# Optimization experiments

Measured on AMD Instinct MI355X. Metric: run time of the kernel, lower is better.

## Reference

```python
import jax, jax.numpy as jnp
from jax import lax
import numpy as np


def _run_lstm(x, W, U, b, reverse=False):
    # x: [B,T,I]; W: [I,4U]; U: [U,4U]; b: [4U]; Keras gate order i,f,g,o
    # activation='relu' (candidate and cell-output), recurrent_activation=sigmoid
    if reverse:
        x = x[:, ::-1]
    u = U.shape[0]
    xz = jnp.einsum('bti,ij->btj', x, W) + b  # precompute input projection

    def step(carry, z_t):
        h, c = carry
        z = z_t + h @ U
        i, f, g, o = jnp.split(z, 4, axis=-1)
        i = jax.nn.sigmoid(i)
        f = jax.nn.sigmoid(f)
        g = jax.nn.relu(g)
        o = jax.nn.sigmoid(o)
        c = f * c + i * g
        h = o * jax.nn.relu(c)
        return (h, c), h

    B = x.shape[0]
    init = (jnp.zeros((B, u), x.dtype), jnp.zeros((B, u), x.dtype))
    _, hs = lax.scan(step, init, jnp.swapaxes(xz, 0, 1))
    hs = jnp.swapaxes(hs, 0, 1)  # [B,T,U]
    if reverse:
        hs = hs[:, ::-1]  # Keras Bidirectional re-reverses backward output
    return hs


def _bilstm(x, Wf, Uf, bf, Wb, Ub, bb):
    return jnp.concatenate([_run_lstm(x, Wf, Uf, bf, False),
                            _run_lstm(x, Wb, Ub, bb, True)], axis=-1)


def _forward(x, p):
    (e1fW, e1fU, e1fb, e1bW, e1bU, e1bb,
     e2fW, e2fU, e2fb, e2bW, e2bU, e2bb,
     d1fW, d1fU, d1fb, d1bW, d1bU, d1bb,
     d2fW, d2fU, d2fb, d2bW, d2bU, d2bb,
     Wd, bd) = p
    T = x.shape[1]
    h = _bilstm(x, e1fW, e1fU, e1fb, e1bW, e1bU, e1bb)          # [B,T,2N]
    # encoder lstm2: return_sequences=False -> last fwd state, last bwd state
    fwd = _run_lstm(h, e2fW, e2fU, e2fb, False)[:, -1]           # [B,N/2]
    bwd = _run_lstm(h, e2bW, e2bU, e2bb, True)[:, 0]             # [B,N/2]
    z = jnp.concatenate([fwd, bwd], axis=-1)                     # [B,N]
    z = jnp.broadcast_to(z[:, None, :], (z.shape[0], T, z.shape[1]))  # RepeatVector
    h = _bilstm(z, d1fW, d1fU, d1fb, d1bW, d1bU, d1bb)           # [B,T,N]
    h = _bilstm(h, d2fW, d2fU, d2fb, d2bW, d2bU, d2bb)           # [B,T,2N]
    return jnp.einsum('btd,df->btf', h, Wd) + bd                 # TimeDistributed Dense


def setup_inputs():
    B, T, F, N = 512, 256, 64, 128
    ks = iter(jax.random.split(jax.random.key(0), 40))

    def p(shape, s=0.05):
        return jax.random.normal(next(ks), shape, jnp.float32) * s

    def cell(ind, u):
        # Keras defaults: zero bias with unit forget-gate bias
        b = jnp.zeros((4 * u,), jnp.float32).at[u:2 * u].set(1.0)
        return p((ind, 4 * u)), p((u, 4 * u)), b

    d = {'x': jax.random.normal(next(ks), (B, T, F), jnp.float32)}
    for name, ind, u in [('e1', F, N), ('e2', 2 * N, N // 2), ('d1', N, N // 2), ('d2', N, N)]:
        for dr in ('f', 'b'):
            W, U, b = cell(ind, u)
            d[name + dr + '_W'] = W
            d[name + dr + '_U'] = U
            d[name + dr + '_b'] = b
    d['Wd'] = p((2 * N, F))
    d['bd'] = jnp.zeros((F,), jnp.float32)
    return d


def reference(x, e1f_W, e1f_U, e1f_b, e1b_W, e1b_U, e1b_b,
              e2f_W, e2f_U, e2f_b, e2b_W, e2b_U, e2b_b,
              d1f_W, d1f_U, d1f_b, d1b_W, d1b_U, d1b_b,
              d2f_W, d2f_U, d2f_b, d2b_W, d2b_U, d2b_b, Wd, bd):
    return _forward(x, (e1f_W, e1f_U, e1f_b, e1b_W, e1b_U, e1b_b,
                        e2f_W, e2f_U, e2f_b, e2b_W, e2b_U, e2b_b,
                        d1f_W, d1f_U, d1f_b, d1b_W, d1b_U, d1b_b,
                        d2f_W, d2f_U, d2f_b, d2b_W, d2b_U, d2b_b, Wd, bd))
```

## Files before the change

### kernel.cpp

```cpp
#include <hip/hip_runtime.h>


#define THREADS 512

using f32x4 = __attribute__((ext_vector_type(4))) float;
using bfrag = __attribute__((ext_vector_type(8))) short;

__device__ __forceinline__ float sigf(float x) { return 1.0f / (1.0f + __expf(-x)); }
__device__ __forceinline__ unsigned short f2bf(float f) {
    unsigned u = __float_as_uint(f);
    u += 0x7FFFu + ((u >> 16) & 1u);
    return (unsigned short)(u >> 16);
}
__device__ __forceinline__ float bf2f(unsigned short h) {
    return __uint_as_float(((unsigned)h) << 16);
}
__device__ __forceinline__ int fragw(int kc, int r) {
    return ((kc * 16 + r) ^ (kc & 7)) * 8;
}

template<int UH, int XK, bool LASTONLY>
__global__ __launch_bounds__(THREADS, 2)
void lstm_rec(const float* __restrict__ xz, const size_t xz_ds, const size_t xz_ss,
              const float* __restrict__ xin,
              const float* __restrict__ Uf, const float* __restrict__ Ub,
              const float* __restrict__ Wf, const float* __restrict__ Wb,
              const float* __restrict__ bf, const float* __restrict__ bb,
              float* __restrict__ out,
              float* __restrict__ stc, float* __restrict__ sth,
              const int T, const int t0, const int TCc, const int FIRST, const int LASTC)
{
    constexpr int NCOL = 4 * UH;
    constexpr int NS   = NCOL / 8;
    constexpr int NT   = NS / 16;
    constexpr int KT   = UH / 32;
    constexpr int XKT  = XK / 32;
    constexpr int PPT  = 16 * UH / THREADS;
    constexpr int BQS  = THREADS / UH;
    constexpr int ZP   = NCOL + 4;
    static_assert(XK == 0 || XK == 64, "x path");
    static_assert(NT >= 1 && KT >= 1 && PPT >= 1, "shape");

    const int dir = blockIdx.y;
    const bool rev = (dir != 0);
    const float* __restrict__ U  = dir ? Ub : Uf;
    const float* __restrict__ Wm = dir ? Wb : Wf;
    const float* __restrict__ bs = dir ? bb : bf;

    const int b0  = blockIdx.x * 16;
    const int tid = threadIdx.x;
    const int wv  = tid >> 6;
    const int l   = tid & 63;
    const int lr  = l & 15;
    const int kg  = l >> 4;
    const int c0  = wv * NS;

    __shared__ unsigned short hh_hi[UH * 16], hh_lo[UH * 16];
    __shared__ unsigned short xh_hi[XK > 0 ? 2 * XK * 16 : 8];
    __shared__ unsigned short xh_lo[XK > 0 ? 2 * XK * 16 : 8];
    __shared__ float zs[16 * ZP];

    bfrag whi[NT][KT], wlo[NT][KT];
    #pragma unroll
    for (int nt = 0; nt < NT; ++nt)
        #pragma unroll
        for (int kt = 0; kt < KT; ++kt) {
            const int col = c0 + nt * 16 + lr;
            #pragma unroll
            for (int i = 0; i < 8; ++i) {
                const int k = kt * 32 + kg * 8 + i;
                const float w = U[(size_t)k * NCOL + col];
                const unsigned short h = f2bf(w);
                whi[nt][kt][i] = (short)h;
                wlo[nt][kt][i] = (short)f2bf(w - bf2f(h));
            }
        }
    bfrag wxhi[NT][XKT > 0 ? XKT : 1];
    float biasr[NT];
    if constexpr (XK > 0) {
        #pragma unroll
        for (int nt = 0; nt < NT; ++nt) {
            const int col = c0 + nt * 16 + lr;
            #pragma unroll
            for (int kt = 0; kt < XKT; ++kt)
                #pragma unroll
                for (int i = 0; i < 8; ++i)
                    wxhi[nt][kt][i] = (short)f2bf(Wm[(size_t)(kt * 32 + kg * 8 + i) * NCOL + col]);
            biasr[nt] = bs[col];
        }
    }

    const int ut = tid % UH;
    float cst[PPT];

    if (FIRST) {
        for (int i = tid; i < UH * 16; i += THREADS) { hh_hi[i] = 0; hh_lo[i] = 0; }
        #pragma unroll
        for (int q = 0; q < PPT; ++q) cst[q] = 0.0f;
    } else {
        #pragma unroll
        for (int q = 0; q < PPT; ++q) {
            const int b = tid / UH + q * BQS;
            const float hv = sth[((size_t)dir * 512 + b0 + b) * UH + ut];
            const unsigned short hi = f2bf(hv);
            const unsigned short lo = f2bf(hv - bf2f(hi));
            hh_hi[fragw(ut >> 3, b) + (ut & 7)] = hi;
            hh_lo[fragw(ut >> 3, b) + (ut & 7)] = lo;
            cst[q] = stc[((size_t)dir * 512 + b0 + b) * UH + ut];
        }
    }
    if constexpr (XK > 0) {
        const int gt0 = rev ? (T - 1 - t0) : t0;
        const int bb = tid >> 5, f = (tid & 31) * 2;
        const float2 xv = *(const float2*)&xin[((size_t)(b0 + bb) * T + gt0) * XK + f];
        const unsigned short h0 = f2bf(xv.x), h1 = f2bf(xv.y);
        const unsigned short l0 = f2bf(xv.x - bf2f(h0)), l1 = f2bf(xv.y - bf2f(h1));
        const int off = fragw(f >> 3, bb) + (f & 7);
        *(unsigned*)&xh_hi[off] = (unsigned)h0 | ((unsigned)h1 << 16);
        *(unsigned*)&xh_lo[off] = (unsigned)l0 | ((unsigned)l1 << 16);
    }
    __syncthreads();

    for (int p = 0; p < TCc; ++p) {
        const int gt = rev ? (T - 1 - (t0 + p)) : (t0 + p);

        float2 xnext;
        const bool havex = (XK > 0) && (p + 1 < TCc);
        if (havex) {
            const int gtn = rev ? (T - 1 - (t0 + p + 1)) : (t0 + p + 1);
            const int bb = tid >> 5, f = (tid & 31) * 2;
            xnext = *(const float2*)&xin[((size_t)(b0 + bb) * T + gtn) * XK + f];
        }
        float xzr[PPT][4];
        if constexpr (XK == 0) {
            const float* xrow = xz + (size_t)dir * xz_ds + (size_t)p * xz_ss;
            #pragma unroll
            for (int q = 0; q < PPT; ++q) {
                const int b = tid / UH + q * BQS;
                const float* r = xrow + (size_t)(b0 + b) * NCOL + ut;
                #pragma unroll
                for (int g = 0; g < 4; ++g) xzr[q][g] = r[g * UH];
            }
        }

        f32x4 acc[NT];
        #pragma unroll
        for (int nt = 0; nt < NT; ++nt) {
            if constexpr (XK > 0) acc[nt] = f32x4{biasr[nt], biasr[nt], biasr[nt], biasr[nt]};
            else                  acc[nt] = f32x4{0.f, 0.f, 0.f, 0.f};
        }
        #pragma unroll
        for (int kt = 0; kt < KT; ++kt) {
            const bfrag ahi = *(const bfrag*)&hh_hi[fragw(kt * 4 + kg, lr)];
            const bfrag alo = *(const bfrag*)&hh_lo[fragw(kt * 4 + kg, lr)];
            #pragma unroll
            for (int nt = 0; nt < NT; ++nt) {
                acc[nt] = __builtin_amdgcn_mfma_f32_16x16x32_bf16(ahi, whi[nt][kt], acc[nt], 0, 0, 0);
                acc[nt] = __builtin_amdgcn_mfma_f32_16x16x32_bf16(alo, whi[nt][kt], acc[nt], 0, 0, 0);
                acc[nt] = __builtin_amdgcn_mfma_f32_16x16x32_bf16(ahi, wlo[nt][kt], acc[nt], 0, 0, 0);
            }
        }
        if constexpr (XK > 0) {
            const int xb = (p & 1) * XK * 16;
            #pragma unroll
            for (int kt = 0; kt < XKT; ++kt) {
                const bfrag xhi = *(const bfrag*)&xh_hi[xb + fragw(kt * 4 + kg, lr)];
                const bfrag xlo = *(const bfrag*)&xh_lo[xb + fragw(kt * 4 + kg, lr)];
                #pragma unroll
                for (int nt = 0; nt < NT; ++nt) {
                    acc[nt] = __builtin_amdgcn_mfma_f32_16x16x32_bf16(xhi, wxhi[nt][kt], acc[nt], 0, 0, 0);
                    acc[nt] = __builtin_amdgcn_mfma_f32_16x16x32_bf16(xlo, wxhi[nt][kt], acc[nt], 0, 0, 0);
                }
            }
        }
        #pragma unroll
        for (int nt = 0; nt < NT; ++nt)
            #pragma unroll
            for (int qq = 0; qq < 4; ++qq)
                zs[(kg * 4 + qq) * ZP + c0 + nt * 16 + lr] = acc[nt][qq];

        __syncthreads();

        if (havex) {
            const int bb = tid >> 5, f = (tid & 31) * 2;
            const unsigned short h0 = f2bf(xnext.x), h1 = f2bf(xnext.y);
            const unsigned short l0 = f2bf(xnext.x - bf2f(h0)), l1 = f2bf(xnext.y - bf2f(h1));
            const int off = ((p + 1) & 1) * XK * 16 + fragw(f >> 3, bb) + (f & 7);
            *(unsigned*)&xh_hi[off] = (unsigned)h0 | ((unsigned)h1 << 16);
            *(unsigned*)&xh_lo[off] = (unsigned)l0 | ((unsigned)l1 << 16);
        }

        #pragma unroll
        for (int q = 0; q < PPT; ++q) {
            const int b = tid / UH + q * BQS;
            float z0 = zs[b * ZP + 0 * UH + ut];
            float z1 = zs[b * ZP + 1 * UH + ut];
            float z2 = zs[b * ZP + 2 * UH + ut];
            float z3 = zs[b * ZP + 3 * UH + ut];
            if constexpr (XK == 0) { z0 += xzr[q][0]; z1 += xzr[q][1]; z2 += xzr[q][2]; z3 += xzr[q][3]; }
            const float iv = sigf(z0);
            const float fv = sigf(z1);
            const float gv = fmaxf(z2, 0.0f);
            const float ov = sigf(z3);
            const float c  = fv * cst[q] + iv * gv;
            cst[q] = c;
            const float h = ov * fmaxf(c, 0.0f);
            if (!LASTONLY) {
                out[((size_t)(b0 + b) * T + gt) * (2 * UH) + (size_t)dir * UH + ut] = h;
            } else if (LASTC && p == TCc - 1) {
                out[(size_t)(b0 + b) * (2 * UH) + (size_t)dir * UH + ut] = h;
            }
            const unsigned short hi = f2bf(h);
            const unsigned short lo = f2bf(h - bf2f(hi));
            hh_hi[fragw(ut >> 3, b) + (ut & 7)] = hi;
            hh_lo[fragw(ut >> 3, b) + (ut & 7)] = lo;
        }
        __syncthreads();
    }

    #pragma unroll
    for (int q = 0; q < PPT; ++q) {
        const int b = tid / UH + q * BQS;
        const float hv = bf2f(hh_hi[fragw(ut >> 3, b) + (ut & 7)])
                       + bf2f(hh_lo[fragw(ut >> 3, b) + (ut & 7)]);
        sth[((size_t)dir * 512 + b0 + b) * UH + ut] = hv;
        stc[((size_t)dir * 512 + b0 + b) * UH + ut] = cst[q];
    }
}

template<int K, int NC, bool TMAP>
__global__ __launch_bounds__(256, 2)
void xz_gemm(const float* __restrict__ A,
             const float* __restrict__ Wf, const float* __restrict__ Wb,
             const float* __restrict__ bf, const float* __restrict__ bb,
             float* __restrict__ xz, const int T, const int t0, const int TC)
{
    const int dir = blockIdx.z;
    const float* __restrict__ W = dir ? Wb : Wf;
    const float* __restrict__ bs = dir ? bb : bf;
    const int row0 = blockIdx.x * 64;
    const int col0 = blockIdx.y * 64;
    const int tid = threadIdx.x;
    const int tx = tid & 15, ty = tid >> 4;

    __shared__ float As[64][17];
    __shared__ float Bs[16][64];

    float acc[4][4];
    #pragma unroll
    for (int i = 0; i < 4; ++i)
        #pragma unroll
        for (int j = 0; j < 4; ++j) acc[i][j] = 0.0f;

    const int r_st = tid >> 2;
    const int kq   = (tid & 3) * 4;
    const int rowA = row0 + r_st;
    const float* Arow;
    if (TMAP) {
        const int ltA = rowA >> 9, bA = rowA & 511;
        const int gtA = dir ? (T - 1 - (t0 + ltA)) : (t0 + ltA);
        Arow = A + ((size_t)bA * T + gtA) * K;
    } else {
        Arow = A + (size_t)rowA * K;
    }
    const int kr = tid >> 4, c4 = (tid & 15) * 4;

    for (int kc = 0; kc < K; kc += 16) {
        *(float4*)&As[r_st][kq] = *(const float4*)&Arow[kc + kq];
        *(float4*)&Bs[kr][c4]   = *(const float4*)&W[(size_t)(kc + kr) * NC + col0 + c4];
        __syncthreads();
        #pragma unroll
        for (int kk = 0; kk < 16; ++kk) {
            float a[4];
            #pragma unroll
            for (int i = 0; i < 4; ++i) a[i] = As[ty * 4 + i][kk];
            const float4 bv = *(const float4*)&Bs[kk][tx * 4];
            #pragma unroll
            for (int i = 0; i < 4; ++i) {
                acc[i][0] = fmaf(a[i], bv.x, acc[i][0]);
                acc[i][1] = fmaf(a[i], bv.y, acc[i][1]);
                acc[i][2] = fmaf(a[i], bv.z, acc[i][2]);
                acc[i][3] = fmaf(a[i], bv.w, acc[i][3]);
            }
        }
        __syncthreads();
    }
    const float4 bv = *(const float4*)&bs[col0 + tx * 4];
    #pragma unroll
    for (int i = 0; i < 4; ++i) {
        const int row = row0 + ty * 4 + i;
        float4 o;
        o.x = acc[i][0] + bv.x; o.y = acc[i][1] + bv.y;
        o.z = acc[i][2] + bv.z; o.w = acc[i][3] + bv.w;
        if (TMAP) {
            const int lt = row >> 9, b = row & 511;
            *(float4*)&xz[(((size_t)dir * TC + lt) * 512 + b) * NC + col0 + tx * 4] = o;
        } else {
            *(float4*)&xz[((size_t)dir * 512 + row) * NC + col0 + tx * 4] = o;
        }
    }
}

__global__ __launch_bounds__(256, 1)
void dense_out(const float* __restrict__ h, const float* __restrict__ Wd,
               const float* __restrict__ bd, float* __restrict__ out, const int rows)
{
    const int tid = threadIdx.x;
    const int lc  = (tid & 15) * 4;
    const size_t row = (size_t)blockIdx.x * 16 + (tid >> 4);
    if (row >= (size_t)rows) return;
    const float* hr = h + row * 256;
    float4 a;
    a.x = bd[lc]; a.y = bd[lc + 1]; a.z = bd[lc + 2]; a.w = bd[lc + 3];
    #pragma unroll 4
    for (int k = 0; k < 256; k += 4) {
        const float4 hv = *reinterpret_cast<const float4*>(&hr[k]);
        const float4 w0 = *reinterpret_cast<const float4*>(&Wd[(size_t)(k + 0) * 64 + lc]);
        const float4 w1 = *reinterpret_cast<const float4*>(&Wd[(size_t)(k + 1) * 64 + lc]);
        const float4 w2 = *reinterpret_cast<const float4*>(&Wd[(size_t)(k + 2) * 64 + lc]);
        const float4 w3 = *reinterpret_cast<const float4*>(&Wd[(size_t)(k + 3) * 64 + lc]);
        a.x = fmaf(hv.x, w0.x, a.x); a.y = fmaf(hv.x, w0.y, a.y); a.z = fmaf(hv.x, w0.z, a.z); a.w = fmaf(hv.x, w0.w, a.w);
        a.x = fmaf(hv.y, w1.x, a.x); a.y = fmaf(hv.y, w1.y, a.y); a.z = fmaf(hv.y, w1.z, a.z); a.w = fmaf(hv.y, w1.w, a.w);
        a.x = fmaf(hv.z, w2.x, a.x); a.y = fmaf(hv.z, w2.y, a.y); a.z = fmaf(hv.z, w2.z, a.z); a.w = fmaf(hv.z, w2.w, a.w);
        a.x = fmaf(hv.w, w3.x, a.x); a.y = fmaf(hv.w, w3.y, a.y); a.z = fmaf(hv.w, w3.z, a.z); a.w = fmaf(hv.w, w3.w, a.w);
    }
    *reinterpret_cast<float4*>(&out[row * 64 + lc]) = a;
}

extern "C" void kernel_launch(void* const* d_in, const int* in_sizes, int n_in,
                              void* d_out, int out_size, void* d_ws, size_t ws_size,
                              hipStream_t stream)
{
    (void)in_sizes; (void)n_in; (void)out_size;
    constexpr int B = 512, T = 256;

    const size_t n_h1 = (size_t)B * T * 256;
    const size_t n_h2 = (size_t)B * T * 128;
    const size_t n_z  = (size_t)B * 128;
    const size_t n_st = 2 * ((size_t)2 * B * 64) + 2 * ((size_t)2 * B * 128);
    const size_t base = n_h1 + n_h2 + n_z + n_st;
    int TC = 0;
    for (int tc : {64, 32, 16}) {
        if ((base + (size_t)tc * 2 * B * 512) * sizeof(float) <= ws_size) { TC = tc; break; }
    }
    if (!TC) return;
    const int NCH = T / TC;

    const float* x    = (const float*)d_in[0];
    const float* e1fW = (const float*)d_in[1];
    const float* e1fU = (const float*)d_in[2];
    const float* e1fb = (const float*)d_in[3];
    const float* e1bW = (const float*)d_in[4];
    const float* e1bU = (const float*)d_in[5];
    const float* e1bb = (const float*)d_in[6];
    const float* e2fW = (const float*)d_in[7];
    const float* e2fU = (const float*)d_in[8];
    const float* e2fb = (const float*)d_in[9];
    const float* e2bW = (const float*)d_in[10];
    const float* e2bU = (const float*)d_in[11];
    const float* e2bb = (const float*)d_in[12];
    const float* d1fW = (const float*)d_in[13];
    const float* d1fU = (const float*)d_in[14];
    const float* d1fb = (const float*)d_in[15];
    const float* d1bW = (const float*)d_in[16];
    const float* d1bU = (const float*)d_in[17];
    const float* d1bb = (const float*)d_in[18];
    const float* d2fW = (const float*)d_in[19];
    const float* d2fU = (const float*)d_in[20];
    const float* d2fb = (const float*)d_in[21];
    const float* d2bW = (const float*)d_in[22];
    const float* d2bU = (const float*)d_in[23];
    const float* d2bb = (const float*)d_in[24];
    const float* Wd   = (const float*)d_in[25];
    const float* bd   = (const float*)d_in[26];
    float* out = (float*)d_out;

    float* ws   = (float*)d_ws;
    float* h1   = ws;
    float* h2   = h1 + n_h1;
    float* zv   = h2 + n_h2;
    float* st   = zv + n_z;
    float* stcE = st;
    float* sthE = stcE + (size_t)2 * B * 64;
    float* stcD = sthE + (size_t)2 * B * 64;
    float* sthD = stcD + (size_t)2 * B * 128;
    float* xzb  = st + n_st;
    float* xzd1 = xzb;
    float* h3   = h1;

    const dim3 rgrid(B / 16, 2), rblk(THREADS);

    lstm_rec<128, 64, false><<<rgrid, rblk, 0, stream>>>(
        nullptr, 0, 0, x, e1fU, e1bU, e1fW, e1bW, e1fb, e1bb,
        h1, stcD, sthD, T, 0, T, 1, 1);

    for (int c = 0; c < NCH; ++c) {
        xz_gemm<256, 256, true><<<dim3(TC * B / 64, 256 / 64, 2), 256, 0, stream>>>(
            h1, e2fW, e2bW, e2fb, e2bb, xzb, T, c * TC, TC);
        lstm_rec<64, 0, true><<<rgrid, rblk, 0, stream>>>(
            xzb, (size_t)TC * 512 * 256, (size_t)512 * 256, nullptr,
            e2fU, e2bU, nullptr, nullptr, nullptr, nullptr,
            zv, stcE, sthE, T, c * TC, TC, c == 0, c == NCH - 1);
    }

    xz_gemm<128, 256, false><<<dim3(B / 64, 256 / 64, 2), 256, 0, stream>>>(
        zv, d1fW, d1bW, d1fb, d1bb, xzd1, T, 0, 1);
    lstm_rec<64, 0, false><<<rgrid, rblk, 0, stream>>>(
        xzd1, (size_t)512 * 256, 0, nullptr,
        d1fU, d1bU, nullptr, nullptr, nullptr, nullptr,
        h2, stcE, sthE, T, 0, T, 1, 1);

    for (int c = 0; c < NCH; ++c) {
        xz_gemm<128, 512, true><<<dim3(TC * B / 64, 512 / 64, 2), 256, 0, stream>>>(
            h2, d2fW, d2bW, d2fb, d2bb, xzb, T, c * TC, TC);
        lstm_rec<128, 0, false><<<rgrid, rblk, 0, stream>>>(
            xzb, (size_t)TC * 512 * 512, (size_t)512 * 512, nullptr,
            d2fU, d2bU, nullptr, nullptr, nullptr, nullptr,
            h3, stcD, sthD, T, c * TC, TC, c == 0, c == NCH - 1);
    }

    dense_out<<<(B * T + 15) / 16, 256, 0, stream>>>(h3, Wd, bd, out, B * T);
}
```

Measured before the change: 3.389 ms.

## Interleave gate columns per wave and double-buffer hidden state to drop a barrier

The recurrent weight columns are permuted so each wave's MFMA output holds all four gates for its own hidden units. Each wave can then do the gate math from a private LDS scratch tile without a block-wide barrier between matmul and activation. The hidden-state LDS buffers are double-buffered so only one __syncthreads per timestep is needed. Launch bounds drop to one block per SM, trading occupancy for registers and LDS.

```diff
diff --git a/kernel.cpp b/kernel.cpp
--- a/kernel.cpp
+++ b/kernel.cpp
@@ -20,7 +20,7 @@
 }
 
 template<int UH, int XK, bool LASTONLY>
-__global__ __launch_bounds__(THREADS, 2)
+__global__ __launch_bounds__(THREADS, 1)
 void lstm_rec(const float* __restrict__ xz, const size_t xz_ds, const size_t xz_ss,
               const float* __restrict__ xin,
               const float* __restrict__ Uf, const float* __restrict__ Ub,
@@ -35,11 +35,12 @@
     constexpr int NT   = NS / 16;
     constexpr int KT   = UH / 32;
     constexpr int XKT  = XK / 32;
-    constexpr int PPT  = 16 * UH / THREADS;
-    constexpr int BQS  = THREADS / UH;
-    constexpr int ZP   = NCOL + 4;
+    constexpr int UPW  = NS / 4;
+    constexpr int PPW  = NT;
+    constexpr int BRW  = 64 / UPW;
+    constexpr int ZPITCH = NS + 4;
     static_assert(XK == 0 || XK == 64, "x path");
-    static_assert(NT >= 1 && KT >= 1 && PPT >= 1, "shape");
+    static_assert(NT >= 1 && KT >= 1 && UPW >= 1, "shape");
 
     const int dir = blockIdx.y;
     const bool rev = (dir != 0);
@@ -55,58 +56,62 @@
     const int kg  = l >> 4;
     const int c0  = wv * NS;
 
-    __shared__ unsigned short hh_hi[UH * 16], hh_lo[UH * 16];
+    __shared__ unsigned short hh_hi[2][UH * 16], hh_lo[2][UH * 16];
     __shared__ unsigned short xh_hi[XK > 0 ? 2 * XK * 16 : 8];
     __shared__ unsigned short xh_lo[XK > 0 ? 2 * XK * 16 : 8];
-    __shared__ float zs[16 * ZP];
+    __shared__ float zw[8][16][ZPITCH];
 
     bfrag whi[NT][KT], wlo[NT][KT];
     #pragma unroll
-    for (int nt = 0; nt < NT; ++nt)
-        #pragma unroll
-        for (int kt = 0; kt < KT; ++kt) {
-            const int col = c0 + nt * 16 + lr;
+    for (int nt = 0; nt < NT; ++nt) {
+        const int colp = c0 + nt * 16 + lr;
+        const int ocol = (colp & 3) * UH + (colp >> 2);
+        #pragma unroll
+        for (int kt = 0; kt < KT; ++kt)
             #pragma unroll
             for (int i = 0; i < 8; ++i) {
                 const int k = kt * 32 + kg * 8 + i;
-                const float w = U[(size_t)k * NCOL + col];
+                const float w = U[(size_t)k * NCOL + ocol];
                 const unsigned short h = f2bf(w);
                 whi[nt][kt][i] = (short)h;
                 wlo[nt][kt][i] = (short)f2bf(w - bf2f(h));
             }
-        }
+    }
     bfrag wxhi[NT][XKT > 0 ? XKT : 1];
     float biasr[NT];
     if constexpr (XK > 0) {
         #pragma unroll
         for (int nt = 0; nt < NT; ++nt) {
-            const int col = c0 + nt * 16 + lr;
+            const int colp = c0 + nt * 16 + lr;
+            const int ocol = (colp & 3) * UH + (colp >> 2);
             #pragma unroll
             for (int kt = 0; kt < XKT; ++kt)
                 #pragma unroll
                 for (int i = 0; i < 8; ++i)
-                    wxhi[nt][kt][i] = (short)f2bf(Wm[(size_t)(kt * 32 + kg * 8 + i) * NCOL + col]);
-            biasr[nt] = bs[col];
-        }
-    }
-
-    const int ut = tid % UH;
-    float cst[PPT];
+                    wxhi[nt][kt][i] = (short)f2bf(Wm[(size_t)(kt * 32 + kg * 8 + i) * NCOL + ocol]);
+            biasr[nt] = bs[ocol];
+        }
+    }
+
+    const int u_loc = l % UPW;
+    const int uu    = wv * UPW + u_loc;
+    const int brow0 = l / UPW;
+    float cst[PPW];
 
     if (FIRST) {
-        for (int i = tid; i < UH * 16; i += THREADS) { hh_hi[i] = 0; hh_lo[i] = 0; }
-        #pragma unroll
-        for (int q = 0; q < PPT; ++q) cst[q] = 0.0f;
+        for (int i = tid; i < UH * 16; i += THREADS) { hh_hi[0][i] = 0; hh_lo[0][i] = 0; }
+        #pragma unroll
+        for (int j = 0; j < PPW; ++j) cst[j] = 0.0f;
     } else {
         #pragma unroll
-        for (int q = 0; q < PPT; ++q) {
-            const int b = tid / UH + q * BQS;
-            const float hv = sth[((size_t)dir * 512 + b0 + b) * UH + ut];
+        for (int j = 0; j < PPW; ++j) {
+            const int b = brow0 + j * BRW;
+            const float hv = sth[((size_t)dir * 512 + b0 + b) * UH + uu];
             const unsigned short hi = f2bf(hv);
             const unsigned short lo = f2bf(hv - bf2f(hi));
-            hh_hi[fragw(ut >> 3, b) + (ut & 7)] = hi;
-            hh_lo[fragw(ut >> 3, b) + (ut & 7)] = lo;
-            cst[q] = stc[((size_t)dir * 512 + b0 + b) * UH + ut];
+            hh_hi[0][fragw(uu >> 3, b) + (uu & 7)] = hi;
+            hh_lo[0][fragw(uu >> 3, b) + (uu & 7)] = lo;
+            cst[j] = stc[((size_t)dir * 512 + b0 + b) * UH + uu];
         }
     }
     if constexpr (XK > 0) {
@@ -122,7 +127,8 @@
     __syncthreads();
 
     for (int p = 0; p < TCc; ++p) {
-        const int gt = rev ? (T - 1 - (t0 + p)) : (t0 + p);
+        const int gt  = rev ? (T - 1 - (t0 + p)) : (t0 + p);
+        const int cur = p & 1, nxt = cur ^ 1;
 
         float2 xnext;
         const bool havex = (XK > 0) && (p + 1 < TCc);
@@ -131,15 +137,15 @@
             const int bb = tid >> 5, f = (tid & 31) * 2;
             xnext = *(const float2*)&xin[((size_t)(b0 + bb) * T + gtn) * XK + f];
         }
-        float xzr[PPT][4];
+        float xzr[PPW][4];
         if constexpr (XK == 0) {
             const float* xrow = xz + (size_t)dir * xz_ds + (size_t)p * xz_ss;
             #pragma unroll
-            for (int q = 0; q < PPT; ++q) {
-                const int b = tid / UH + q * BQS;
-                const float* r = xrow + (size_t)(b0 + b) * NCOL + ut;
+            for (int j = 0; j < PPW; ++j) {
+                const int b = brow0 + j * BRW;
+                const float* r = xrow + (size_t)(b0 + b) * NCOL + uu;
                 #pragma unroll
-                for (int g = 0; g < 4; ++g) xzr[q][g] = r[g * UH];
+                for (int g = 0; g < 4; ++g) xzr[j][g] = r[g * UH];
             }
         }
 
@@ -151,8 +157,8 @@
         }
         #pragma unroll
         for (int kt = 0; kt < KT; ++kt) {
-            const bfrag ahi = *(const bfrag*)&hh_hi[fragw(kt * 4 + kg, lr)];
-            const bfrag alo = *(const bfrag*)&hh_lo[fragw(kt * 4 + kg, lr)];
+            const bfrag ahi = *(const bfrag*)&hh_hi[cur][fragw(kt * 4 + kg, lr)];
+            const bfrag alo = *(const bfrag*)&hh_lo[cur][fragw(kt * 4 + kg, lr)];
             #pragma unroll
             for (int nt = 0; nt < NT; ++nt) {
                 acc[nt] = __builtin_amdgcn_mfma_f32_16x16x32_bf16(ahi, whi[nt][kt], acc[nt], 0, 0, 0);
@@ -161,7 +167,7 @@
             }
         }
         if constexpr (XK > 0) {
-            const int xb = (p & 1) * XK * 16;
+            const int xb = cur * XK * 16;
             #pragma unroll
             for (int kt = 0; kt < XKT; ++kt) {
                 const bfrag xhi = *(const bfrag*)&xh_hi[xb + fragw(kt * 4 + kg, lr)];
@@ -173,58 +179,60 @@
                 }
             }
         }
+
         #pragma unroll
         for (int nt = 0; nt < NT; ++nt)
             #pragma unroll
             for (int qq = 0; qq < 4; ++qq)
-                zs[(kg * 4 + qq) * ZP + c0 + nt * 16 + lr] = acc[nt][qq];
-
-        __syncthreads();
+                zw[wv][kg * 4 + qq][nt * 16 + lr] = acc[nt][qq];
+        __asm__ __volatile__("s_waitcnt lgkmcnt(0)" ::: "memory");
+        __builtin_amdgcn_sched_barrier(0);
+
+        #pragma unroll
+        for (int j = 0; j < PPW; ++j) {
+            const int b = brow0 + j * BRW;
+            float4 z4 = *(const float4*)&zw[wv][b][u_loc * 4];
+            if constexpr (XK == 0) {
+                z4.x += xzr[j][0]; z4.y += xzr[j][1]; z4.z += xzr[j][2]; z4.w += xzr[j][3];
+            }
+            const float iv = sigf(z4.x);
+            const float fv = sigf(z4.y);
+            const float gv = fmaxf(z4.z, 0.0f);
+            const float ov = sigf(z4.w);
+            const float c  = fv * cst[j] + iv * gv;
+            cst[j] = c;
+            const float h = ov * fmaxf(c, 0.0f);
+            if (!LASTONLY) {
+                out[((size_t)(b0 + b) * T + gt) * (2 * UH) + (size_t)dir * UH + uu] = h;
+            } else if (LASTC && p == TCc - 1) {
+                out[(size_t)(b0 + b) * (2 * UH) + (size_t)dir * UH + uu] = h;
+            }
+            const unsigned short hi = f2bf(h);
+            const unsigned short lo = f2bf(h - bf2f(hi));
+            hh_hi[nxt][fragw(uu >> 3, b) + (uu & 7)] = hi;
+            hh_lo[nxt][fragw(uu >> 3, b) + (uu & 7)] = lo;
+        }
 
         if (havex) {
             const int bb = tid >> 5, f = (tid & 31) * 2;
             const unsigned short h0 = f2bf(xnext.x), h1 = f2bf(xnext.y);
             const unsigned short l0 = f2bf(xnext.x - bf2f(h0)), l1 = f2bf(xnext.y - bf2f(h1));
-            const int off = ((p + 1) & 1) * XK * 16 + fragw(f >> 3, bb) + (f & 7);
+            const int off = nxt * XK * 16 + fragw(f >> 3, bb) + (f & 7);
             *(unsigned*)&xh_hi[off] = (unsigned)h0 | ((unsigned)h1 << 16);
             *(unsigned*)&xh_lo[off] = (unsigned)l0 | ((unsigned)l1 << 16);
         }
 
-        #pragma unroll
-        for (int q = 0; q < PPT; ++q) {
-            const int b = tid / UH + q * BQS;
-            float z0 = zs[b * ZP + 0 * UH + ut];
-            float z1 = zs[b * ZP + 1 * UH + ut];
-            float z2 = zs[b * ZP + 2 * UH + ut];
-            float z3 = zs[b * ZP + 3 * UH + ut];
-            if constexpr (XK == 0) { z0 += xzr[q][0]; z1 += xzr[q][1]; z2 += xzr[q][2]; z3 += xzr[q][3]; }
-            const float iv = sigf(z0);
-            const float fv = sigf(z1);
-            const float gv = fmaxf(z2, 0.0f);
-            const float ov = sigf(z3);
-            const float c  = fv * cst[q] + iv * gv;
-            cst[q] = c;
-            const float h = ov * fmaxf(c, 0.0f);
-            if (!LASTONLY) {
-                out[((size_t)(b0 + b) * T + gt) * (2 * UH) + (size_t)dir * UH + ut] = h;
-            } else if (LASTC && p == TCc - 1) {
-                out[(size_t)(b0 + b) * (2 * UH) + (size_t)dir * UH + ut] = h;
-            }
-            const unsigned short hi = f2bf(h);
-            const unsigned short lo = f2bf(h - bf2f(hi));
-            hh_hi[fragw(ut >> 3, b) + (ut & 7)] = hi;
-            hh_lo[fragw(ut >> 3, b) + (ut & 7)] = lo;
-        }
         __syncthreads();
     }
 
+    const int fin = TCc & 1;
     #pragma unroll
-    for (int q = 0; q < PPT; ++q) {
-        const int b = tid / UH + q * BQS;
-        const float hv = bf2f(hh_hi[fragw(ut >> 3, b) + (ut & 7)])
-                       + bf2f(hh_lo[fragw(ut >> 3, b) + (ut & 7)]);
-        sth[((size_t)dir * 512 + b0 + b) * UH + ut] = hv;
-        stc[((size_t)dir * 512 + b0 + b) * UH + ut] = cst[q];
+    for (int j = 0; j < PPW; ++j) {
+        const int b = brow0 + j * BRW;
+        const float hv = bf2f(hh_hi[fin][fragw(uu >> 3, b) + (uu & 7)])
+                       + bf2f(hh_lo[fin][fragw(uu >> 3, b) + (uu & 7)]);
+        sth[((size_t)dir * 512 + b0 + b) * UH + uu] = hv;
+        stc[((size_t)dir * 512 + b0 + b) * UH + uu] = cst[j];
     }
 }
 
```

Result: no change. 3.426 ms (+1.1%).
